# Kernel optimization log

Measured on AMD Instinct MI355X. Metric: run time of the kernel, lower is better.

## Reference

```python
import jax, jax.numpy as jnp
import numpy as np

B = 128          # batch of initial states
NUM_TRAJ = 128   # noise realizations per state
D = 16           # state dim (output_dim)
P = 5            # number of physical params
H = 64           # hidden width of the tiny drift/diffusion MLPs
DELTAT = 2.0 ** -8
MAXT = 0.25
STEPS = int(round(MAXT / DELTAT)) - 1   # 63 Euler-Maruyama steps (tvec has 64 points)
F = 1 + 2 * D + P                        # NN feature dim: [t, Re(x), Im(x), params]
N = B * NUM_TRAJ                         # total trajectories after tiling


def setup_inputs() -> dict:
    key = jax.random.key(0)
    ks = jax.random.split(key, 8)
    x_real = jax.random.normal(ks[0], (B, D), jnp.float32)
    x_imag = jax.random.normal(ks[1], (B, D), jnp.float32)
    params = jax.random.uniform(ks[2], (P,), jnp.float32)
    # Brownian increments dW ~ N(0, deltat), m=1 noise channel
    noise = jax.random.normal(ks[3], (N, STEPS, 1), jnp.float32) * float(np.sqrt(DELTAT))
    # Stacked weights for the 4 nets: [a_real, a_imag, b_real, b_imag]
    W1 = jax.random.normal(ks[4], (4, F, H), jnp.float32) / np.float32(np.sqrt(F))
    B1 = jax.random.normal(ks[5], (4, H), jnp.float32) * 0.01
    W2 = jax.random.normal(ks[6], (4, H, D), jnp.float32) / np.float32(np.sqrt(H)) * 0.5
    B2 = jax.random.normal(ks[7], (4, D), jnp.float32) * 0.01
    return {"x_real": x_real, "x_imag": x_imag, "params": params, "noise": noise,
            "W1": W1, "B1": B1, "W2": W2, "B2": B2}


def reference(x_real, x_imag, params, noise, W1, B1, W2, B2):
    # call(): tile params over batch, tile state over num_traj (input_param=-1 path)
    x = jax.lax.complex(x_real, x_imag)          # [B, D] complex64
    x = jnp.tile(x, (NUM_TRAJ, 1))               # [N, D]
    p = jnp.broadcast_to(params[None, :], (N, P))  # traj_inputs

    dt = jnp.float32(DELTAT)
    tvec = jnp.arange(STEPS, dtype=jnp.float32) * dt       # t_n for each Euler step
    dWs = jnp.swapaxes(noise, 0, 1)                          # [STEPS, N, 1]

    def nets(t, x):
        # NN drift/diffusion: features [t, Re(x), Im(x), params] -> 4 tiny MLPs at once
        feats = jnp.concatenate(
            [jnp.broadcast_to(t, (N, 1)), x.real, x.imag, p], axis=1)  # [N, F]
        h = jnp.tanh(jnp.einsum('nf,kfh->knh', feats, W1) + B1[:, None, :])
        o = jnp.einsum('knh,khd->knd', h, W2) + B2[:, None, :]          # [4, N, D]
        a = jax.lax.complex(o[0], o[1])   # drift,     [N, D]
        b = jax.lax.complex(o[2], o[3])   # diffusion, [N, D] (m=1)
        return a, b

    def step(x, inp):
        t, dw = inp                        # dw: [N, 1] real
        a, b = nets(t, x)
        x_next = x + a * dt + b * dw       # Euler-Maruyama
        return x_next, None

    xT, _ = jax.lax.scan(step, x, (tvec, dWs))
    # return final state y = xvec[:, -1] as concatenated real/imag parts [N, 2D]
    return jnp.concatenate([xT.real, xT.imag], axis=-1)
```

## Files before the change

### kernel.cpp

```cpp
#include <hip/hip_runtime.h>
#include <stdint.h>

#define NB    128
#define NSTEP 63
#define DT    0.00390625f
#define TSC   2.8853900817779268f

typedef __attribute__((ext_vector_type(8))) short bf16x8;
typedef __attribute__((ext_vector_type(4))) float f32x4;
typedef __attribute__((ext_vector_type(2))) float f32x2;

union Frag { bf16x8 v; uint32_t u[4]; };

__device__ __forceinline__ short f2bf(float f) {
    uint32_t u = __float_as_uint(f);
    u += 0x7FFF + ((u >> 16) & 1);
    return (short)(u >> 16);
}

__device__ __forceinline__ uint32_t pk_bf16(float lo, float hi) {
    uint32_t r;
    asm("v_cvt_pk_bf16_f32 %0, %1, %2" : "=v"(r) : "v"(lo), "v"(hi));
    return r;
}

__device__ __forceinline__ f32x2 tanh2_sc(float y0, float y1) {
    f32x2 e = { __builtin_amdgcn_exp2f(y0), __builtin_amdgcn_exp2f(y1) };
    f32x2 ep = e + (f32x2)1.0f;
    f32x2 r = { __builtin_amdgcn_rcpf(ep.x), __builtin_amdgcn_rcpf(ep.y) };
    return __builtin_elementwise_fma(r, (f32x2)(-2.0f), (f32x2)(1.0f));
}

__global__ __launch_bounds__(256, 1) void sde_1wave(
    const float* __restrict__ x_real, const float* __restrict__ x_imag,
    const float* __restrict__ params, const float* __restrict__ noise,
    const float* __restrict__ W1, const float* __restrict__ B1,
    const float* __restrict__ W2, const float* __restrict__ B2,
    float* __restrict__ out)
{
    const int tid  = threadIdx.x;
    const int lane = tid & 63;
    const int l15  = lane & 15;
    const int g    = lane >> 4;
    const int wv   = tid >> 6;
    const int wid  = blockIdx.x * 4 + wv;
    const int n    = wid * 16 + l15;

    Frag w1f[16];
    #pragma unroll
    for (int t = 0; t < 16; ++t) {
        const int net = t >> 2;
        const int hn  = 16 * (t & 3) + l15;
        #pragma unroll
        for (int j = 0; j < 8; ++j) {
            const int jf = (j < 4) ? (4 * g + j) : (16 + 4 * g + (j - 4));
            w1f[t].v[j] = f2bf(TSC * W1[(net * 38 + 1 + jf) * 64 + hn]);
        }
    }

    Frag w2f[4][2];
    #pragma unroll
    for (int k = 0; k < 4; ++k)
        #pragma unroll
        for (int kt = 0; kt < 2; ++kt)
            #pragma unroll
            for (int j = 0; j < 8; ++j) {
                const int hl = 16 * (2 * kt + (j >> 2)) + 4 * g + (j & 3);
                w2f[k][kt].v[j] = f2bf(W2[(k * 64 + hl) * 16 + l15]);
            }

    float pr[5];
    #pragma unroll
    for (int p = 0; p < 5; ++p) pr[p] = params[p];
    f32x4 biascur[16], wtdt[16];
    #pragma unroll
    for (int t = 0; t < 16; ++t) {
        #pragma unroll
        for (int r = 0; r < 4; ++r) {
            const int c1 = 16 * t + 4 * g + r;
            const int net = c1 >> 6, h = c1 & 63;
            float b = B1[net * 64 + h];
            #pragma unroll
            for (int p = 0; p < 5; ++p)
                b = fmaf(pr[p], W1[(net * 38 + 33 + p) * 64 + h], b);
            biascur[t][r] = TSC * b;
            wtdt[t][r]    = (TSC * DT) * W1[(net * 38 + 0) * 64 + h];
        }
    }

    f32x4 bc[4];
    #pragma unroll
    for (int k = 0; k < 4; ++k)
        #pragma unroll
        for (int r = 0; r < 4; ++r) bc[k][r] = B2[k * 16 + 4 * g + r];

    const int xrow = n & (NB - 1);
    f32x4 sre = *reinterpret_cast<const f32x4*>(&x_real[xrow * 16 + 4 * g]);
    f32x4 sim = *reinterpret_cast<const f32x4*>(&x_imag[xrow * 16 + 4 * g]);

    const float* __restrict__ nsp = noise + (size_t)n * NSTEP;
    float dw = nsp[0];

    for (int s = 0; s < NSTEP; ++s) {
        const float dwn = nsp[(s + 1 < NSTEP) ? s + 1 : s];

        Frag bx;
        bx.u[0] = pk_bf16(sre[0], sre[1]);
        bx.u[1] = pk_bf16(sre[2], sre[3]);
        bx.u[2] = pk_bf16(sim[0], sim[1]);
        bx.u[3] = pk_bf16(sim[2], sim[3]);

        f32x4 acc[16];
        #pragma unroll
        for (int t = 0; t < 16; ++t)
            acc[t] = __builtin_amdgcn_mfma_f32_16x16x32_bf16(
                w1f[t].v, bx.v, biascur[t], 0, 0, 0);
        #pragma unroll
        for (int t = 0; t < 16; ++t) biascur[t] += wtdt[t];

        f32x4 th[16];
        #pragma unroll
        for (int t = 0; t < 16; ++t) {
            const f32x2 lo = tanh2_sc(acc[t][0], acc[t][1]);
            const f32x2 hi = tanh2_sc(acc[t][2], acc[t][3]);
            th[t][0] = lo.x; th[t][1] = lo.y; th[t][2] = hi.x; th[t][3] = hi.y;
        }

        f32x4 o[4];
        #pragma unroll
        for (int k = 0; k < 4; ++k) {
            o[k] = bc[k];
            #pragma unroll
            for (int kt = 0; kt < 2; ++kt) {
                const int T0 = 4 * k + 2 * kt;
                Frag pb;
                pb.u[0] = pk_bf16(th[T0][0],     th[T0][1]);
                pb.u[1] = pk_bf16(th[T0][2],     th[T0][3]);
                pb.u[2] = pk_bf16(th[T0 + 1][0], th[T0 + 1][1]);
                pb.u[3] = pk_bf16(th[T0 + 1][2], th[T0 + 1][3]);
                o[k] = __builtin_amdgcn_mfma_f32_16x16x32_bf16(
                    w2f[k][kt].v, pb.v, o[k], 0, 0, 0);
            }
        }

        const f32x4 dt4 = (f32x4)DT;
        const f32x4 dw4 = (f32x4)dw;
        sre = __builtin_elementwise_fma(dt4, o[0],
              __builtin_elementwise_fma(dw4, o[2], sre));
        sim = __builtin_elementwise_fma(dt4, o[1],
              __builtin_elementwise_fma(dw4, o[3], sim));
        dw = dwn;
    }

    *reinterpret_cast<f32x4*>(out + (size_t)n * 32 + 4 * g)      = sre;
    *reinterpret_cast<f32x4*>(out + (size_t)n * 32 + 16 + 4 * g) = sim;
}

extern "C" void kernel_launch(void* const* d_in, const int* in_sizes, int n_in,
                              void* d_out, int out_size, void* d_ws, size_t ws_size,
                              hipStream_t stream) {
    const float* x_real = (const float*)d_in[0];
    const float* x_imag = (const float*)d_in[1];
    const float* params = (const float*)d_in[2];
    const float* noise  = (const float*)d_in[3];
    const float* W1     = (const float*)d_in[4];
    const float* B1     = (const float*)d_in[5];
    const float* W2     = (const float*)d_in[6];
    const float* B2     = (const float*)d_in[7];
    float* out = (float*)d_out;

    sde_1wave<<<dim3(256), dim3(256), 0, stream>>>(
        x_real, x_imag, params, noise, W1, B1, W2, B2, out);
}
```

Baseline: 85.07 us.

## Split the four nets across two waves per 16-trajectory tile, use Padé tanh

Each block of two waves now handles 16 trajectories. Wave 0 computes the drift nets and wave 1 the diffusion nets, and the two exchange their second-layer outputs through double-buffered LDS with a barrier every step. This halves each wave's serial MFMA and tanh chain and launches 4x more waves (1024 blocks of 128 threads), raising parallelism on the 256 CUs. The exp2/rcp tanh is replaced by a clamped [7/6]-style Padé rational, which trades the exp for a few FMAs but adds approximation error. The per-step __syncthreads adds sync cost.

```diff
diff --git a/kernel.cpp b/kernel.cpp
--- a/kernel.cpp
+++ b/kernel.cpp
@@ -4,7 +4,6 @@
 #define NB    128
 #define NSTEP 63
 #define DT    0.00390625f
-#define TSC   2.8853900817779268f
 
 typedef __attribute__((ext_vector_type(8))) short bf16x8;
 typedef __attribute__((ext_vector_type(4))) float f32x4;
@@ -24,75 +23,80 @@
     return r;
 }
 
-__device__ __forceinline__ f32x2 tanh2_sc(float y0, float y1) {
-    f32x2 e = { __builtin_amdgcn_exp2f(y0), __builtin_amdgcn_exp2f(y1) };
-    f32x2 ep = e + (f32x2)1.0f;
-    f32x2 r = { __builtin_amdgcn_rcpf(ep.x), __builtin_amdgcn_rcpf(ep.y) };
-    return __builtin_elementwise_fma(r, (f32x2)(-2.0f), (f32x2)(1.0f));
+__device__ __forceinline__ f32x2 tanh2_pade(f32x2 x) {
+    f32x2 xc = __builtin_elementwise_min(
+                   __builtin_elementwise_max(x, (f32x2)(-4.0f)), (f32x2)(4.0f));
+    f32x2 z   = xc * xc;
+    f32x2 num = __builtin_elementwise_fma(z + (f32x2)105.0f, z, (f32x2)945.0f) * xc;
+    f32x2 den = __builtin_elementwise_fma(z, (f32x2)15.0f, (f32x2)420.0f);
+    den       = __builtin_elementwise_fma(den, z, (f32x2)945.0f);
+    f32x2 r = { __builtin_amdgcn_rcpf(den.x), __builtin_amdgcn_rcpf(den.y) };
+    return num * r;
 }
 
-__global__ __launch_bounds__(256, 1) void sde_1wave(
+__global__ __launch_bounds__(128, 2) void sde_2wave(
     const float* __restrict__ x_real, const float* __restrict__ x_imag,
     const float* __restrict__ params, const float* __restrict__ noise,
     const float* __restrict__ W1, const float* __restrict__ B1,
     const float* __restrict__ W2, const float* __restrict__ B2,
     float* __restrict__ out)
 {
+    __shared__ f32x2 xb[2][4][2][64];
+
     const int tid  = threadIdx.x;
     const int lane = tid & 63;
     const int l15  = lane & 15;
     const int g    = lane >> 4;
-    const int wv   = tid >> 6;
-    const int wid  = blockIdx.x * 4 + wv;
-    const int n    = wid * 16 + l15;
+    const int w    = tid >> 6;
+    const int n    = blockIdx.x * 16 + l15;
 
-    Frag w1f[16];
+    Frag w1f[8];
     #pragma unroll
-    for (int t = 0; t < 16; ++t) {
-        const int net = t >> 2;
+    for (int t = 0; t < 8; ++t) {
+        const int net = 2 * w + (t >> 2);
         const int hn  = 16 * (t & 3) + l15;
         #pragma unroll
         for (int j = 0; j < 8; ++j) {
             const int jf = (j < 4) ? (4 * g + j) : (16 + 4 * g + (j - 4));
-            w1f[t].v[j] = f2bf(TSC * W1[(net * 38 + 1 + jf) * 64 + hn]);
+            w1f[t].v[j] = f2bf(W1[(net * 38 + 1 + jf) * 64 + hn]);
         }
     }
 
-    Frag w2f[4][2];
+    Frag w2f[2][2];
     #pragma unroll
-    for (int k = 0; k < 4; ++k)
+    for (int j2 = 0; j2 < 2; ++j2)
         #pragma unroll
         for (int kt = 0; kt < 2; ++kt)
             #pragma unroll
             for (int j = 0; j < 8; ++j) {
                 const int hl = 16 * (2 * kt + (j >> 2)) + 4 * g + (j & 3);
-                w2f[k][kt].v[j] = f2bf(W2[(k * 64 + hl) * 16 + l15]);
+                w2f[j2][kt].v[j] = f2bf(W2[((2 * w + j2) * 64 + hl) * 16 + l15]);
             }
 
     float pr[5];
     #pragma unroll
     for (int p = 0; p < 5; ++p) pr[p] = params[p];
-    f32x4 biascur[16], wtdt[16];
+    f32x4 biascur[8], wtdt[8];
     #pragma unroll
-    for (int t = 0; t < 16; ++t) {
+    for (int t = 0; t < 8; ++t) {
+        const int net = 2 * w + (t >> 2);
         #pragma unroll
         for (int r = 0; r < 4; ++r) {
-            const int c1 = 16 * t + 4 * g + r;
-            const int net = c1 >> 6, h = c1 & 63;
+            const int h = 16 * (t & 3) + 4 * g + r;
             float b = B1[net * 64 + h];
             #pragma unroll
             for (int p = 0; p < 5; ++p)
                 b = fmaf(pr[p], W1[(net * 38 + 33 + p) * 64 + h], b);
-            biascur[t][r] = TSC * b;
-            wtdt[t][r]    = (TSC * DT) * W1[(net * 38 + 0) * 64 + h];
+            biascur[t][r] = b;
+            wtdt[t][r]    = DT * W1[(net * 38 + 0) * 64 + h];
         }
     }
 
-    f32x4 bc[4];
+    f32x4 bc[2];
     #pragma unroll
-    for (int k = 0; k < 4; ++k)
+    for (int j2 = 0; j2 < 2; ++j2)
         #pragma unroll
-        for (int r = 0; r < 4; ++r) bc[k][r] = B2[k * 16 + 4 * g + r];
+        for (int r = 0; r < 4; ++r) bc[j2][r] = B2[(2 * w + j2) * 16 + 4 * g + r];
 
     const int xrow = n & (NB - 1);
     f32x4 sre = *reinterpret_cast<const f32x4*>(&x_real[xrow * 16 + 4 * g]);
@@ -110,50 +114,66 @@
         bx.u[2] = pk_bf16(sim[0], sim[1]);
         bx.u[3] = pk_bf16(sim[2], sim[3]);
 
-        f32x4 acc[16];
+        f32x4 acc[8];
         #pragma unroll
-        for (int t = 0; t < 16; ++t)
+        for (int t = 0; t < 8; ++t)
             acc[t] = __builtin_amdgcn_mfma_f32_16x16x32_bf16(
                 w1f[t].v, bx.v, biascur[t], 0, 0, 0);
         #pragma unroll
-        for (int t = 0; t < 16; ++t) biascur[t] += wtdt[t];
+        for (int t = 0; t < 8; ++t) biascur[t] += wtdt[t];
 
-        f32x4 th[16];
+        f32x4 o[2];
         #pragma unroll
-        for (int t = 0; t < 16; ++t) {
-            const f32x2 lo = tanh2_sc(acc[t][0], acc[t][1]);
-            const f32x2 hi = tanh2_sc(acc[t][2], acc[t][3]);
-            th[t][0] = lo.x; th[t][1] = lo.y; th[t][2] = hi.x; th[t][3] = hi.y;
-        }
-
-        f32x4 o[4];
-        #pragma unroll
-        for (int k = 0; k < 4; ++k) {
-            o[k] = bc[k];
+        for (int j2 = 0; j2 < 2; ++j2) {
+            o[j2] = bc[j2];
             #pragma unroll
             for (int kt = 0; kt < 2; ++kt) {
-                const int T0 = 4 * k + 2 * kt;
+                const int T0 = 4 * j2 + 2 * kt;
+                const f32x2 t0 = tanh2_pade((f32x2){acc[T0][0],     acc[T0][1]});
+                const f32x2 t1 = tanh2_pade((f32x2){acc[T0][2],     acc[T0][3]});
+                const f32x2 t2 = tanh2_pade((f32x2){acc[T0 + 1][0], acc[T0 + 1][1]});
+                const f32x2 t3 = tanh2_pade((f32x2){acc[T0 + 1][2], acc[T0 + 1][3]});
                 Frag pb;
-                pb.u[0] = pk_bf16(th[T0][0],     th[T0][1]);
-                pb.u[1] = pk_bf16(th[T0][2],     th[T0][3]);
-                pb.u[2] = pk_bf16(th[T0 + 1][0], th[T0 + 1][1]);
-                pb.u[3] = pk_bf16(th[T0 + 1][2], th[T0 + 1][3]);
-                o[k] = __builtin_amdgcn_mfma_f32_16x16x32_bf16(
-                    w2f[k][kt].v, pb.v, o[k], 0, 0, 0);
+                pb.u[0] = pk_bf16(t0.x, t0.y);  pb.u[1] = pk_bf16(t1.x, t1.y);
+                pb.u[2] = pk_bf16(t2.x, t2.y);  pb.u[3] = pk_bf16(t3.x, t3.y);
+                o[j2] = __builtin_amdgcn_mfma_f32_16x16x32_bf16(
+                    w2f[j2][kt].v, pb.v, o[j2], 0, 0, 0);
             }
         }
 
+        const int db = s & 1;
+        xb[db][0][w][lane] = (f32x2){o[0][0], o[0][1]};
+        xb[db][1][w][lane] = (f32x2){o[0][2], o[0][3]};
+        xb[db][2][w][lane] = (f32x2){o[1][0], o[1][1]};
+        xb[db][3][w][lane] = (f32x2){o[1][2], o[1][3]};
+        __syncthreads();
+        const f32x2 q0 = xb[db][0][w ^ 1][lane];
+        const f32x2 q1 = xb[db][1][w ^ 1][lane];
+        const f32x2 q2 = xb[db][2][w ^ 1][lane];
+        const f32x2 q3 = xb[db][3][w ^ 1][lane];
+        const f32x4 oth0 = {q0.x, q0.y, q1.x, q1.y};
+        const f32x4 oth1 = {q2.x, q2.y, q3.x, q3.y};
+
         const f32x4 dt4 = (f32x4)DT;
         const f32x4 dw4 = (f32x4)dw;
-        sre = __builtin_elementwise_fma(dt4, o[0],
-              __builtin_elementwise_fma(dw4, o[2], sre));
-        sim = __builtin_elementwise_fma(dt4, o[1],
-              __builtin_elementwise_fma(dw4, o[3], sim));
+        if (w == 0) {
+            sre = __builtin_elementwise_fma(dt4, o[0],
+                  __builtin_elementwise_fma(dw4, oth0, sre));
+            sim = __builtin_elementwise_fma(dt4, o[1],
+                  __builtin_elementwise_fma(dw4, oth1, sim));
+        } else {
+            sre = __builtin_elementwise_fma(dt4, oth0,
+                  __builtin_elementwise_fma(dw4, o[0], sre));
+            sim = __builtin_elementwise_fma(dt4, oth1,
+                  __builtin_elementwise_fma(dw4, o[1], sim));
+        }
         dw = dwn;
     }
 
-    *reinterpret_cast<f32x4*>(out + (size_t)n * 32 + 4 * g)      = sre;
-    *reinterpret_cast<f32x4*>(out + (size_t)n * 32 + 16 + 4 * g) = sim;
+    if (w == 0) {
+        *reinterpret_cast<f32x4*>(out + (size_t)n * 32 + 4 * g)      = sre;
+        *reinterpret_cast<f32x4*>(out + (size_t)n * 32 + 16 + 4 * g) = sim;
+    }
 }
 
 extern "C" void kernel_launch(void* const* d_in, const int* in_sizes, int n_in,
@@ -169,6 +189,6 @@
     const float* B2     = (const float*)d_in[7];
     float* out = (float*)d_out;
 
-    sde_1wave<<<dim3(256), dim3(256), 0, stream>>>(
+    sde_2wave<<<dim3(1024), dim3(128), 0, stream>>>(
         x_real, x_imag, params, noise, W1, B1, W2, B2, out);
 }
```

New measurement: 108.8 us. 1.28x slower.
